# Kernel optimization log

Measured on AMD Instinct MI355X. Metric: run time of the kernel, lower is better.

Reference implementation:

```python
import jax, jax.numpy as jnp
import numpy as np

SEQ, B, N_IN, H, L = 8192, 1, 64, 1024, 5


def leaky_relu(x):
    return jnp.where(x >= 0, x, 0.01 * x)  # torch LeakyReLU default slope 0.01


def setup_inputs() -> dict:
    key = jax.random.key(0)
    ks = jax.random.split(key, 6)
    s_in = 1.0 / np.sqrt(N_IN)
    s_h = 1.0 / np.sqrt(H)
    return {
        "data_in": jax.random.normal(ks[0], (SEQ, B, N_IN), jnp.float32),
        "w1": jax.random.normal(ks[1], (H, N_IN), jnp.float32) * s_in,
        "b1": jnp.zeros((H,), jnp.float32),
        "W_ih": jax.random.normal(ks[2], (L, 4 * H, H), jnp.float32) * s_h,
        "W_hh": jax.random.normal(ks[3], (L, 4 * H, H), jnp.float32) * s_h,
        "b_ih": jnp.zeros((L, 4 * H), jnp.float32),
        "b_hh": jnp.zeros((L, 4 * H), jnp.float32),
        "w2": jax.random.normal(ks[4], (N_IN, H), jnp.float32) * s_h,
        "b2": jnp.zeros((N_IN,), jnp.float32),
        "h0": jnp.zeros((L, B, H), jnp.float32),
        "c0": jnp.zeros((L, B, H), jnp.float32),
    }


def _lstm_layer(x, h0, c0, Wih, Whh, b):
    # x: (SEQ, B, H_in); h0, c0: (B, H); Wih: (4H, H_in); Whh: (4H, H); b: (4H,)
    def step(carry, x_t):
        h, c = carry
        z = x_t @ Wih.T + h @ Whh.T + b  # (B, 4H)
        i, f, g, o = jnp.split(z, 4, axis=-1)  # torch gate order i,f,g,o
        i = jax.nn.sigmoid(i)
        f = jax.nn.sigmoid(f)
        g = jnp.tanh(g)
        o = jax.nn.sigmoid(o)
        c = f * c + i * g
        h = o * jnp.tanh(c)
        return (h, c), h

    (_, _), hs = jax.lax.scan(step, (h0, c0), x)
    return hs  # (SEQ, B, H)


def reference(data_in, w1, b1, W_ih, W_hh, b_ih, b_hh, w2, b2, h0, c0):
    out = leaky_relu(data_in @ w1.T + b1)  # (SEQ, B, H)
    for l in range(W_ih.shape[0]):  # stacked LSTM, layers is a static small int
        out = _lstm_layer(out, h0[l], c0[l], W_ih[l], W_hh[l], b_ih[l] + b_hh[l])
    out = leaky_relu(out)
    return jnp.tanh(out @ w2.T + b2)  # (SEQ, B, N_IN)
```

## Files before the change

kernel.cpp:

```cpp
#include <hip/hip_runtime.h>
#include <stdint.h>

typedef unsigned int  u32;
typedef unsigned short u16;
typedef unsigned long long u64;

#define SEQ    8192
#define HID    1024
#define NL     5
#define NWG    256
#define TPB    256
#define PAIRS  20
#define RPW    20
#define NVR    12
#define NLR    8
#define WSTEPS (SEQ + NL - 1)
#define LWGS   52
#define RING   16

#define WS_X0    ((size_t)0)
#define WS_H5    ((size_t)16*1024*1024)
#define WS_SLOT  ((size_t)32*1024*1024)
#define WS_SYNC  (WS_SLOT + (size_t)384*1024)
#define WS_NEED  (WS_SYNC + 4096)

__device__ __forceinline__ float bf2f(u16 v) { return __uint_as_float(((u32)v) << 16); }
__device__ __forceinline__ float bflo(u32 v) { return __uint_as_float(v << 16); }
__device__ __forceinline__ float bfhi(u32 v) { return __uint_as_float(v & 0xffff0000u); }

__device__ __forceinline__ u16 f2bf(float f) {
  u32 u = __float_as_uint(f);
  u32 r = u + 0x7fffu + ((u >> 16) & 1u);
  return (u16)(r >> 16);
}
__device__ __forceinline__ float lrelu(float x) { return (x >= 0.f) ? x : 0.01f * x; }
__device__ __forceinline__ float sigm(float x)  { return 1.f / (1.f + __expf(-x)); }
__device__ __forceinline__ float tanh_f(float x) {
  float e = __expf(-2.f * fabsf(x));
  float t = (1.f - e) / (1.f + e);
  return (x >= 0.f) ? t : -t;
}

__device__ __forceinline__ float dot2bf(u32 w, u32 v, float acc) {
  return fmaf(bfhi(w), bfhi(v), fmaf(bflo(w), bflo(v), acc));
}

#if defined(__has_builtin)
#if __has_builtin(__builtin_amdgcn_fdot2_f32_bf16)
#define HAS_DOT2 1
typedef __bf16 bf16x2 __attribute__((ext_vector_type(2)));
__device__ __forceinline__ float hwdot2(u32 a, u32 b, float c) {
  union U { u32 u; bf16x2 v; };
  U x, y; x.u = a; y.u = b;
  return __builtin_amdgcn_fdot2_f32_bf16(x.v, y.v, c, false);
}
#endif
#endif
#ifndef HAS_DOT2
#define HAS_DOT2 0
__device__ __forceinline__ float hwdot2(u32 a, u32 b, float c) { return dot2bf(a, b, c); }
#endif

__device__ __forceinline__ u32 agent_load(const u32* p) {
  return __hip_atomic_load((u32*)p, __ATOMIC_RELAXED, __HIP_MEMORY_SCOPE_AGENT);
}
__device__ __forceinline__ u64 slot_load(const u64* p) {
  return __hip_atomic_load((u64*)p, __ATOMIC_RELAXED, __HIP_MEMORY_SCOPE_AGENT);
}
__device__ __forceinline__ void slot_store(u64* p, u64 v) {
  __hip_atomic_store(p, v, __ATOMIC_RELAXED, __HIP_MEMORY_SCOPE_AGENT);
}
__device__ __forceinline__ void epoch_add(u32* p) {
  (void)__hip_atomic_fetch_add(p, 1u, __ATOMIC_RELAXED, __HIP_MEMORY_SCOPE_AGENT);
}

__global__ void k_detect(const u32* __restrict__ w1, u32* __restrict__ flag) {
  int lane = threadIdx.x;
  int cnt = 0;
#pragma unroll
  for (int i = 0; i < 4; ++i) {
    u32 w = w1[lane * 4 + i];
    u32 e = (w >> 23) & 0xffu;
    cnt += (e >= 100u && e <= 140u) ? 1 : 0;
  }
  cnt += __shfl_xor(cnt, 32); cnt += __shfl_xor(cnt, 16); cnt += __shfl_xor(cnt, 8);
  cnt += __shfl_xor(cnt, 4);  cnt += __shfl_xor(cnt, 2);  cnt += __shfl_xor(cnt, 1);
  if (lane == 0) {
    u32 f = (cnt > 128) ? 1u : 0u;
#if HAS_DOT2
    u32 a1 = (u32)f2bf(1.5f)   | ((u32)f2bf(-2.25f) << 16);
    u32 b1v = (u32)f2bf(0.5f)  | ((u32)f2bf(4.0f)   << 16);
    u32 a2 = (u32)f2bf(0.125f) | ((u32)f2bf(3.0f)   << 16);
    u32 b2v = (u32)f2bf(8.0f)  | ((u32)f2bf(-0.5f)  << 16);
    float t1 = hwdot2(a1, b1v, 1.0f);
    float t2 = hwdot2(a2, b2v, 0.5f);
    if (fabsf(t1 + 7.25f) < 1e-2f && fabsf(t2) < 1e-2f) f |= 2u;
#endif
    *flag = f;
  }
}

__global__ void __launch_bounds__(256) k_in(const void* __restrict__ din,
                                            const void* __restrict__ w1,
                                            const void* __restrict__ b1,
                                            u32* __restrict__ X0,
                                            const u32* __restrict__ flagp) {
  const u32 isf = *flagp & 1u;
  int t = blockIdx.x, tid = threadIdx.x;
  __shared__ float xs[64];
  if (isf) {
    if (tid < 64) xs[tid] = ((const float*)din)[(size_t)t * 64 + tid];
  } else {
    if (tid < 32) {
      u32 v = ((const u32*)din)[(size_t)t * 32 + tid];
      xs[2 * tid] = bflo(v); xs[2 * tid + 1] = bfhi(v);
    }
  }
  __syncthreads();
  float o[4];
#pragma unroll
  for (int r = 0; r < 4; ++r) {
    int i = tid * 4 + r;
    float a = 0.f;
    if (isf) {
      const float* wr = (const float*)w1 + (size_t)i * 64;
#pragma unroll
      for (int d = 0; d < 64; ++d) a = fmaf(wr[d], xs[d], a);
      a += ((const float*)b1)[i];
    } else {
      const u32* wr = (const u32*)w1 + (size_t)i * 32;
#pragma unroll
      for (int d = 0; d < 32; ++d) {
        u32 w = wr[d];
        a = fmaf(bflo(w), xs[2 * d], a);
        a = fmaf(bfhi(w), xs[2 * d + 1], a);
      }
      a += bf2f(((const u16*)b1)[i]);
    }
    o[r] = lrelu(a);
  }
  X0[(size_t)t * 512 + tid * 2]     = (u32)f2bf(o[0]) | ((u32)f2bf(o[1]) << 16);
  X0[(size_t)t * 512 + tid * 2 + 1] = (u32)f2bf(o[2]) | ((u32)f2bf(o[3]) << 16);
}

__global__ void __launch_bounds__(TPB, 1) k_wave(const void* __restrict__ WihP,
                                                 const void* __restrict__ WhhP,
                                                 const void* __restrict__ bihP,
                                                 const void* __restrict__ bhhP,
                                                 const void* __restrict__ h0P,
                                                 const void* __restrict__ c0P,
                                                 const u32* __restrict__ X0,
                                                 u32* __restrict__ H5,
                                                 u64* slots64, u32* epochs,
                                                 const u32* __restrict__ flagp) {
  const u32 dfl = *flagp;
  const u32 isf = dfl & 1u;
  const bool ud2 = (dfl & 2u) != 0u;
  const int tid  = threadIdx.x;
  const int lane = tid & 63;
  const int wv   = tid >> 6;
  const int wg   = blockIdx.x;

  __shared__ u32   vlds[2][64 * 17];
  __shared__ u32   wlds[4 * NLR * 1024];
  __shared__ float zrow[80];

  u32 W[NVR][16];
#pragma unroll
  for (int i = 0; i < RPW; ++i) {
    int rr = wv * RPW + i;
    int p = rr >> 2, q = rr & 3;
    int g = wg * PAIRS + p;
    int lg = g >> 10, j = g & 1023;
    u32 tmp[16];
    if (isf) {
      const float* matf = (lane < 32) ? (const float*)WihP : (const float*)WhhP;
      const float4* s4 = (const float4*)(matf + ((size_t)(lg * 4096 + q * 1024 + j)) * 1024 + (lane & 31) * 32);
#pragma unroll
      for (int q4 = 0; q4 < 8; ++q4) {
        float4 f = s4[q4];
        tmp[q4 * 2]     = (u32)f2bf(f.x) | ((u32)f2bf(f.y) << 16);
        tmp[q4 * 2 + 1] = (u32)f2bf(f.z) | ((u32)f2bf(f.w) << 16);
      }
    } else {
      const u32* mat = (lane < 32) ? (const u32*)WihP : (const u32*)WhhP;
      const uint4* s4 = (const uint4*)(mat + ((size_t)(lg * 4096 + q * 1024 + j)) * 512 + (lane & 31) * 16);
      uint4 a0 = s4[0], a1 = s4[1], a2 = s4[2], a3 = s4[3];
      tmp[0]=a0.x; tmp[1]=a0.y; tmp[2]=a0.z;  tmp[3]=a0.w;
      tmp[4]=a1.x; tmp[5]=a1.y; tmp[6]=a1.z;  tmp[7]=a1.w;
      tmp[8]=a2.x; tmp[9]=a2.y; tmp[10]=a2.z; tmp[11]=a2.w;
      tmp[12]=a3.x;tmp[13]=a3.y;tmp[14]=a3.z; tmp[15]=a3.w;
    }
    if (i < NVR) {
#pragma unroll
      for (int d = 0; d < 16; ++d) W[i][d] = tmp[d];
    } else {
      u32* base = &wlds[(wv * NLR + (i - NVR)) * 1024];
#pragma unroll
      for (int d4 = 0; d4 < 4; ++d4) {
        uint4 v4 = make_uint4(tmp[d4*4], tmp[d4*4+1], tmp[d4*4+2], tmp[d4*4+3]);
        *(uint4*)&base[d4 * 256 + lane * 4] = v4;
      }
    }
  }

  float cst = 0.f;
  float b0 = 0.f, b1g = 0.f, b2g = 0.f, b3g = 0.f;
  if (wv == 0 && lane < PAIRS) {
    int g = wg * PAIRS + lane, lg = g >> 10, j = g & 1023;
    cst = isf ? ((const float*)c0P)[lg * 1024 + j] : bf2f(((const u16*)c0P)[lg * 1024 + j]);
#pragma unroll
    for (int q = 0; q < 4; ++q) {
      int r = lg * 4096 + q * 1024 + j;
      float bb = isf ? (((const float*)bihP)[r] + ((const float*)bhhP)[r])
                     : (bf2f(((const u16*)bihP)[r]) + bf2f(((const u16*)bhhP)[r]));
      if (q == 0) b0 = bb; else if (q == 1) b1g = bb; else if (q == 2) b2g = bb; else b3g = bb;
    }
  }
  if (tid < PAIRS / 2) {
    int g = wg * PAIRS + 2 * tid, lg = g >> 10, j = g & 1023;
    u32 v;
    if (isf) {
      const float* h0f = (const float*)h0P;
      v = (u32)f2bf(h0f[lg * 1024 + j]) | ((u32)f2bf(h0f[lg * 1024 + j + 1]) << 16);
    } else {
      const u16* h0b = (const u16*)h0P;
      v = (u32)h0b[lg * 1024 + j] | ((u32)h0b[lg * 1024 + j + 1] << 16);
    }
    slot_store(&slots64[(size_t)(lg * RING + (RING - 1)) * 512 + (j >> 1)],
               ((u64)0xFFFFFFFFull << 32) | (u64)v);
  }

  const int l_lo = (wg * PAIRS) >> 10;
  const int l_hi = (wg * PAIRS + PAIRS - 1) >> 10;

  int budget = 20000000;

  for (int s = 0; s < WSTEPS; ++s) {
#pragma unroll
    for (int sel = 0; sel < 2; ++sel) {
      int L = l_lo + sel;
      if (L <= l_hi) {
        int t = s - L;
        if (t >= 0 && t < SEQ) {
          const u64* hsrc = slots64 + (size_t)(L * RING + ((t - 1) & (RING - 1))) * 512;
          const u64* xsrc = (L > 0) ? slots64 + (size_t)((L - 1) * RING + (t & (RING - 1))) * 512
                                    : (const u64*)0;
          const u32 exph = (u32)(t - 1);
          const u32 expx = (u32)t;
          u32 okm = 0;
          u32 dat[4] = {0u, 0u, 0u, 0u};
          int miss = 0;
          for (;;) {
#pragma unroll
            for (int rr2 = 0; rr2 < 4; ++rr2) {
              if (!(okm & (1u << rr2))) {
                int gidx = tid + rr2 * 256;
                if (gidx < 512) {
                  if (L == 0) { dat[rr2] = X0[(size_t)t * 512 + gidx]; okm |= 1u << rr2; }
                  else {
                    u64 v = slot_load(xsrc + gidx);
                    if ((u32)(v >> 32) == expx) { dat[rr2] = (u32)v; okm |= 1u << rr2; }
                  }
                } else {
                  u64 v = slot_load(hsrc + (gidx - 512));
                  if ((u32)(v >> 32) == exph) { dat[rr2] = (u32)v; okm |= 1u << rr2; }
                }
              }
            }
            if (__all(okm == 15u)) break;
            if (--budget < 0) break;
            if (++miss >= 16) __builtin_amdgcn_s_sleep(1);
          }
#pragma unroll
          for (int rr2 = 0; rr2 < 4; ++rr2) {
            int gidx = tid + rr2 * 256;
            vlds[sel][(gidx >> 4) * 17 + (gidx & 15)] = dat[rr2];
          }
        }
      }
    }
    __syncthreads();

    {
      int curl = -1;
      u32 vreg[16];
#pragma unroll
      for (int i = 0; i < RPW; ++i) {
        int rr = wv * RPW + i;
        int p = rr >> 2;
        int g = wg * PAIRS + p;
        int lg = g >> 10;
        int t = s - lg;
        if (t >= 0 && t < SEQ) {
          if (lg != curl) {
            curl = lg;
            const u32* vb = &vlds[lg - l_lo][lane * 17];
#pragma unroll
            for (int d = 0; d < 16; ++d) vreg[d] = vb[d];
          }
          float a0 = 0.f, a1 = 0.f, a2 = 0.f, a3 = 0.f;
          if (i < NVR) {
            if (ud2) {
#pragma unroll
              for (int d = 0; d < 16; d += 4) {
                a0 = hwdot2(W[i][d],   vreg[d],   a0);
                a1 = hwdot2(W[i][d+1], vreg[d+1], a1);
                a2 = hwdot2(W[i][d+2], vreg[d+2], a2);
                a3 = hwdot2(W[i][d+3], vreg[d+3], a3);
              }
            } else {
#pragma unroll
              for (int d = 0; d < 16; d += 4) {
                a0 = fmaf(bflo(W[i][d]),   bflo(vreg[d]),   a0);
                a0 = fmaf(bfhi(W[i][d]),   bfhi(vreg[d]),   a0);
                a1 = fmaf(bflo(W[i][d+1]), bflo(vreg[d+1]), a1);
                a1 = fmaf(bfhi(W[i][d+1]), bfhi(vreg[d+1]), a1);
                a2 = fmaf(bflo(W[i][d+2]), bflo(vreg[d+2]), a2);
                a2 = fmaf(bfhi(W[i][d+2]), bfhi(vreg[d+2]), a2);
                a3 = fmaf(bflo(W[i][d+3]), bflo(vreg[d+3]), a3);
                a3 = fmaf(bfhi(W[i][d+3]), bfhi(vreg[d+3]), a3);
              }
            }
          } else {
            const uint4* wl = (const uint4*)&wlds[(wv * NLR + (i - NVR)) * 1024 + lane * 4];
#pragma unroll
            for (int d4 = 0; d4 < 4; ++d4) {
              uint4 w4 = wl[d4 * 64];
              if (ud2) {
                a0 = hwdot2(w4.x, vreg[d4*4+0], a0);
                a1 = hwdot2(w4.y, vreg[d4*4+1], a1);
                a2 = hwdot2(w4.z, vreg[d4*4+2], a2);
                a3 = hwdot2(w4.w, vreg[d4*4+3], a3);
              } else {
                a0 = fmaf(bflo(w4.x), bflo(vreg[d4*4+0]), a0);
                a0 = fmaf(bfhi(w4.x), bfhi(vreg[d4*4+0]), a0);
                a1 = fmaf(bflo(w4.y), bflo(vreg[d4*4+1]), a1);
                a1 = fmaf(bfhi(w4.y), bfhi(vreg[d4*4+1]), a1);
                a2 = fmaf(bflo(w4.z), bflo(vreg[d4*4+2]), a2);
                a2 = fmaf(bfhi(w4.z), bfhi(vreg[d4*4+2]), a2);
                a3 = fmaf(bflo(w4.w), bflo(vreg[d4*4+3]), a3);
                a3 = fmaf(bfhi(w4.w), bfhi(vreg[d4*4+3]), a3);
              }
            }
          }
          float r = (a0 + a1) + (a2 + a3);
          r += __shfl_xor(r, 32);
          r += __shfl_xor(r, 16);
          r += __shfl_xor(r, 8);
          r += __shfl_xor(r, 4);
          r += __shfl_xor(r, 2);
          r += __shfl_xor(r, 1);
          if (lane == 0) zrow[rr] = r;
        }
      }
    }
    __syncthreads();

    if (wv == 0) {
      if (s >= RING - 1) {
        u32 needw = 52u * (u32)(s - (RING - 2));
#pragma unroll
        for (int sel = 0; sel < 2; ++sel) {
          int L = l_lo + sel;
          if (L <= l_hi && (L + 1) < NL) {
            int tL = s - L;
            if (tL >= 0 && tL < SEQ) {
              while (agent_load(&epochs[(L + 1) * 32]) < needw) {
                if (--budget < 0) break;
                __builtin_amdgcn_s_sleep(4);
              }
            }
          }
        }
      }
      u16 hb = 0;
      int g = wg * PAIRS + lane;
      int lg = g >> 10;
      int t = s - lg;
      bool act = (lane < PAIRS) && (t >= 0) && (t < SEQ);
      if (act) {
        float zi = zrow[lane * 4 + 0] + b0;
        float zf = zrow[lane * 4 + 1] + b1g;
        float zg = zrow[lane * 4 + 2] + b2g;
        float zo = zrow[lane * 4 + 3] + b3g;
        float ig = sigm(zi), fg = sigm(zf), gg = tanh_f(zg), og = sigm(zo);
        float c = fg * cst + ig * gg;
        cst = c;
        hb = f2bf(og * tanh_f(c));
      }
      u16 hnb = (u16)__shfl_xor((int)hb, 1);
      if (act && ((lane & 1) == 0)) {
        int j = g & 1023;
        u32 v = (u32)hb | ((u32)hnb << 16);
        slot_store(&slots64[(size_t)(lg * RING + (t & (RING - 1))) * 512 + (j >> 1)],
                   ((u64)(u32)t << 32) | (u64)v);
        if (lg == NL - 1) H5[(size_t)t * 512 + (j >> 1)] = v;
      }
      if (lane == 0) {
        epoch_add(&epochs[l_lo * 32]);
        if (l_hi != l_lo) epoch_add(&epochs[l_hi * 32]);
      }
    }
  }
}

__global__ void __launch_bounds__(256) k_out(const u32* __restrict__ H5,
                                             const void* __restrict__ w2,
                                             const void* __restrict__ b2,
                                             void* __restrict__ out,
                                             const u32* __restrict__ flagp) {
  const u32 isf = *flagp & 1u;
  int t = blockIdx.x, tid = threadIdx.x;
  __shared__ float hs[1024];
  __shared__ float part[256];
#pragma unroll
  for (int r = 0; r < 2; ++r) {
    int idx = tid + r * 256;
    u32 v = H5[(size_t)t * 512 + idx];
    hs[2 * idx]     = lrelu(bflo(v));
    hs[2 * idx + 1] = lrelu(bfhi(v));
  }
  __syncthreads();
  int n = tid & 63, qq = tid >> 6;
  float a = 0.f;
  if (isf) {
    const float* wr = (const float*)w2 + (size_t)n * 1024 + qq * 256;
    const float* hb = &hs[qq * 256];
#pragma unroll
    for (int d = 0; d < 256; ++d) a = fmaf(wr[d], hb[d], a);
  } else {
    const u32* wr = (const u32*)w2 + (size_t)n * 512 + qq * 128;
    const float* hb = &hs[qq * 256];
#pragma unroll
    for (int d = 0; d < 128; ++d) {
      u32 w = wr[d];
      a = fmaf(bflo(w), hb[2 * d], a);
      a = fmaf(bfhi(w), hb[2 * d + 1], a);
    }
  }
  part[tid] = a;
  __syncthreads();
  if (tid < 64) {
    float bb = isf ? ((const float*)b2)[tid] : bf2f(((const u16*)b2)[tid]);
    float y = part[tid] + part[tid + 64] + part[tid + 128] + part[tid + 192] + bb;
    float r = tanh_f(y);
    if (isf) ((float*)out)[(size_t)t * 64 + tid] = r;
    else     ((u16*)out)[(size_t)t * 64 + tid] = f2bf(r);
  }
}

extern "C" void kernel_launch(void* const* d_in, const int* in_sizes, int n_in,
                              void* d_out, int out_size, void* d_ws, size_t ws_size,
                              hipStream_t stream) {
  (void)in_sizes; (void)n_in; (void)out_size;
  if (ws_size < WS_NEED) return;

  const void* din = d_in[0];
  const void* w1  = d_in[1];
  const void* b1  = d_in[2];
  const void* Wih = d_in[3];
  const void* Whh = d_in[4];
  const void* bih = d_in[5];
  const void* bhh = d_in[6];
  const void* w2  = d_in[7];
  const void* b2  = d_in[8];
  const void* h0  = d_in[9];
  const void* c0  = d_in[10];

  char* ws = (char*)d_ws;
  u32* X0     = (u32*)(ws + WS_X0);
  u32* H5     = (u32*)(ws + WS_H5);
  u64* slot   = (u64*)(ws + WS_SLOT);
  u32* epochs = (u32*)(ws + WS_SYNC);
  u32* dflag  = (u32*)(ws + WS_SYNC + 2048);

  hipMemsetAsync(slot, 0xAA, (size_t)NL * RING * 512 * 8, stream);
  hipMemsetAsync(epochs, 0, 4096, stream);
  k_detect<<<1, 64, 0, stream>>>((const u32*)w1, dflag);
  k_in  <<<SEQ, 256, 0, stream>>>(din, w1, b1, X0, dflag);
  k_wave<<<NWG, TPB, 0, stream>>>(Wih, Whh, bih, bhh, h0, c0, X0, H5, slot, epochs, dflag);
  k_out <<<SEQ, 256, 0, stream>>>(H5, w2, b2, d_out, dflag);
}
```

Measured before the change: 103.6 ms.

## Skew layer wavefront by two steps and prefetch inter-layer inputs via LLC-coherent 16B slots

Layers in the persistent LSTM wavefront now trail one another by two steps instead of one, which gives the next layer's input a step of slack. That input is prefetched at the end of each step, so the spin-wait mostly covers only the recurrent h vector. Slots are repacked as 16-byte records (tag plus two bf16 pairs) written and read with sc0 sc1 dwordx4 inline asm, which cuts the number of tagged atomics per step. The write-after-read throttle now caches how far ahead the consumer layer is, so it polls less often. The costs are a few more pipeline fill steps, reliance on hand-written cache-control asm, and subtler ordering assumptions in the ring buffer.

```diff
diff --git a/kernel.cpp b/kernel.cpp
--- a/kernel.cpp
+++ b/kernel.cpp
@@ -14,7 +14,8 @@
 #define RPW    20
 #define NVR    12
 #define NLR    8
-#define WSTEPS (SEQ + NL - 1)
+#define SKEW   2
+#define WSTEPS (SEQ + SKEW * (NL - 1))
 #define LWGS   52
 #define RING   16
 
@@ -23,6 +24,8 @@
 #define WS_SLOT  ((size_t)32*1024*1024)
 #define WS_SYNC  (WS_SLOT + (size_t)384*1024)
 #define WS_NEED  (WS_SYNC + 4096)
+
+#define VIDX(w) ((((w) >> 4) * 17) + ((w) & 15))
 
 __device__ __forceinline__ float bf2f(u16 v) { return __uint_as_float(((u32)v) << 16); }
 __device__ __forceinline__ float bflo(u32 v) { return __uint_as_float(v << 16); }
@@ -64,15 +67,25 @@
 __device__ __forceinline__ u32 agent_load(const u32* p) {
   return __hip_atomic_load((u32*)p, __ATOMIC_RELAXED, __HIP_MEMORY_SCOPE_AGENT);
 }
-__device__ __forceinline__ u64 slot_load(const u64* p) {
-  return __hip_atomic_load((u64*)p, __ATOMIC_RELAXED, __HIP_MEMORY_SCOPE_AGENT);
-}
-__device__ __forceinline__ void slot_store(u64* p, u64 v) {
-  __hip_atomic_store(p, v, __ATOMIC_RELAXED, __HIP_MEMORY_SCOPE_AGENT);
-}
 __device__ __forceinline__ void epoch_add(u32* p) {
   (void)__hip_atomic_fetch_add(p, 1u, __ATOMIC_RELAXED, __HIP_MEMORY_SCOPE_AGENT);
 }
+
+typedef u32 u32x4_t __attribute__((ext_vector_type(4)));
+__device__ __forceinline__ void llc_store4(u32* p, u32 tag, u32 a, u32 b) {
+  u32x4_t q; q.x = tag; q.y = a; q.z = b; q.w = 0u;
+  asm volatile("global_store_dwordx4 %0, %1, off sc0 sc1" : : "v"(p), "v"(q) : "memory");
+}
+__device__ __forceinline__ u32x4_t llc_load4(const u32* p) {
+  u32x4_t r;
+  asm volatile("global_load_dwordx4 %0, %1, off sc0 sc1" : "=v"(r) : "v"(p));
+  return r;
+}
+__device__ __forceinline__ void vm_drain() {
+  asm volatile("s_waitcnt vmcnt(0)" ::: "memory");
+}
+
+__device__ __forceinline__ int first_wg(int l) { return (l << 10) / PAIRS; }
 
 __global__ void k_detect(const u32* __restrict__ w1, u32* __restrict__ flag) {
   int lane = threadIdx.x;
@@ -151,7 +164,7 @@
                                                  const void* __restrict__ c0P,
                                                  const u32* __restrict__ X0,
                                                  u32* __restrict__ H5,
-                                                 u64* slots64, u32* epochs,
+                                                 u32* slots, u32* epochs,
                                                  const u32* __restrict__ flagp) {
   const u32 dfl = *flagp;
   const u32 isf = dfl & 1u;
@@ -217,67 +230,76 @@
       if (q == 0) b0 = bb; else if (q == 1) b1g = bb; else if (q == 2) b2g = bb; else b3g = bb;
     }
   }
-  if (tid < PAIRS / 2) {
-    int g = wg * PAIRS + 2 * tid, lg = g >> 10, j = g & 1023;
-    u32 v;
+  if (tid < 5) {
+    int u = wg * PAIRS + 4 * tid, lg = u >> 10, j = u & 1023;
+    u32 p0, p1;
     if (isf) {
-      const float* h0f = (const float*)h0P;
-      v = (u32)f2bf(h0f[lg * 1024 + j]) | ((u32)f2bf(h0f[lg * 1024 + j + 1]) << 16);
+      const float* h0f = (const float*)h0P + lg * 1024 + j;
+      p0 = (u32)f2bf(h0f[0]) | ((u32)f2bf(h0f[1]) << 16);
+      p1 = (u32)f2bf(h0f[2]) | ((u32)f2bf(h0f[3]) << 16);
     } else {
-      const u16* h0b = (const u16*)h0P;
-      v = (u32)h0b[lg * 1024 + j] | ((u32)h0b[lg * 1024 + j + 1] << 16);
-    }
-    slot_store(&slots64[(size_t)(lg * RING + (RING - 1)) * 512 + (j >> 1)],
-               ((u64)0xFFFFFFFFull << 32) | (u64)v);
+      const u16* h0b = (const u16*)h0P + lg * 1024 + j;
+      p0 = (u32)h0b[0] | ((u32)h0b[1] << 16);
+      p1 = (u32)h0b[2] | ((u32)h0b[3] << 16);
+    }
+    llc_store4(slots + ((size_t)(lg * RING + (RING - 1)) * 256 + (j >> 2)) * 4,
+               0xFFFFFFFFu, p0, p1);
   }
 
   const int l_lo = (wg * PAIRS) >> 10;
   const int l_hi = (wg * PAIRS + PAIRS - 1) >> 10;
+  const bool span = (l_hi != l_lo);
 
   int budget = 20000000;
+  int war_until0 = RING - 1;
+  int war_until1 = RING - 1;
+  bool pf0 = false, pf1 = false;
 
   for (int s = 0; s < WSTEPS; ++s) {
-#pragma unroll
-    for (int sel = 0; sel < 2; ++sel) {
-      int L = l_lo + sel;
-      if (L <= l_hi) {
-        int t = s - L;
-        if (t >= 0 && t < SEQ) {
-          const u64* hsrc = slots64 + (size_t)(L * RING + ((t - 1) & (RING - 1))) * 512;
-          const u64* xsrc = (L > 0) ? slots64 + (size_t)((L - 1) * RING + (t & (RING - 1))) * 512
-                                    : (const u64*)0;
-          const u32 exph = (u32)(t - 1);
-          const u32 expx = (u32)t;
-          u32 okm = 0;
-          u32 dat[4] = {0u, 0u, 0u, 0u};
-          int miss = 0;
-          for (;;) {
-#pragma unroll
-            for (int rr2 = 0; rr2 < 4; ++rr2) {
-              if (!(okm & (1u << rr2))) {
-                int gidx = tid + rr2 * 256;
-                if (gidx < 512) {
-                  if (L == 0) { dat[rr2] = X0[(size_t)t * 512 + gidx]; okm |= 1u << rr2; }
-                  else {
-                    u64 v = slot_load(xsrc + gidx);
-                    if ((u32)(v >> 32) == expx) { dat[rr2] = (u32)v; okm |= 1u << rr2; }
-                  }
-                } else {
-                  u64 v = slot_load(hsrc + (gidx - 512));
-                  if ((u32)(v >> 32) == exph) { dat[rr2] = (u32)v; okm |= 1u << rr2; }
-                }
-              }
-            }
-            if (__all(okm == 15u)) break;
-            if (--budget < 0) break;
-            if (++miss >= 16) __builtin_amdgcn_s_sleep(1);
-          }
-#pragma unroll
-          for (int rr2 = 0; rr2 < 4; ++rr2) {
-            int gidx = tid + rr2 * 256;
-            vlds[sel][(gidx >> 4) * 17 + (gidx & 15)] = dat[rr2];
-          }
-        }
+    const int t0 = s - 2 * l_lo;
+    const int t1 = s - 2 * l_hi;
+    const bool a0 = (t0 >= 0) && (t0 < SEQ);
+    const bool a1 = span && (t1 >= 0) && (t1 < SEQ);
+
+    if (a0 && l_lo == 0) {
+      u64 xv = *(const u64*)(X0 + (size_t)t0 * 512 + 2 * tid);
+      vlds[0][VIDX(2 * tid)]     = (u32)xv;
+      vlds[0][VIDX(2 * tid + 1)] = (u32)(xv >> 32);
+    }
+
+    {
+      bool h0ok = !a0, h1ok = !a1;
+      bool x0ok = !a0 || (l_lo == 0) || pf0;
+      bool x1ok = !a1 || pf1;
+      const u32* ha0 = slots + ((size_t)(l_lo * RING + ((t0 - 1) & 15)) * 256 + tid) * 4;
+      const u32* ha1 = slots + ((size_t)(l_hi * RING + ((t1 - 1) & 15)) * 256 + tid) * 4;
+      const u32* xa0 = (l_lo > 0)
+          ? slots + ((size_t)((l_lo - 1) * RING + (t0 & 15)) * 256 + tid) * 4 : ha0;
+      const u32* xa1 = slots + ((size_t)(l_lo * RING + (t1 & 15)) * 256 + tid) * 4;
+      const u32 eh0 = (u32)(t0 - 1), eh1 = (u32)(t1 - 1);
+      const u32 ex0 = (u32)t0, ex1 = (u32)t1;
+      int miss = 0;
+      while (!__all(h0ok && h1ok && x0ok && x1ok)) {
+        u32x4_t wh0, wh1, wx0, wx1;
+        if (!h0ok) wh0 = llc_load4(ha0);
+        if (!h1ok) wh1 = llc_load4(ha1);
+        if (!x0ok) wx0 = llc_load4(xa0);
+        if (!x1ok) wx1 = llc_load4(xa1);
+        vm_drain();
+        if (!h0ok && wh0.x == eh0) {
+          vlds[0][VIDX(512 + 2 * tid)] = wh0.y; vlds[0][VIDX(513 + 2 * tid)] = wh0.z; h0ok = true;
+        }
+        if (!h1ok && wh1.x == eh1) {
+          vlds[1][VIDX(512 + 2 * tid)] = wh1.y; vlds[1][VIDX(513 + 2 * tid)] = wh1.z; h1ok = true;
+        }
+        if (!x0ok && wx0.x == ex0) {
+          vlds[0][VIDX(2 * tid)] = wx0.y; vlds[0][VIDX(2 * tid + 1)] = wx0.z; x0ok = true;
+        }
+        if (!x1ok && wx1.x == ex1) {
+          vlds[1][VIDX(2 * tid)] = wx1.y; vlds[1][VIDX(2 * tid + 1)] = wx1.z; x1ok = true;
+        }
+        if (--budget < 0) break;
+        if (++miss >= 16) __builtin_amdgcn_s_sleep(1);
       }
     }
     __syncthreads();
@@ -291,7 +313,7 @@
         int p = rr >> 2;
         int g = wg * PAIRS + p;
         int lg = g >> 10;
-        int t = s - lg;
+        int t = s - 2 * lg;
         if (t >= 0 && t < SEQ) {
           if (lg != curl) {
             curl = lg;
@@ -358,26 +380,28 @@
     __syncthreads();
 
     if (wv == 0) {
-      if (s >= RING - 1) {
-        u32 needw = 52u * (u32)(s - (RING - 2));
-#pragma unroll
-        for (int sel = 0; sel < 2; ++sel) {
-          int L = l_lo + sel;
-          if (L <= l_hi && (L + 1) < NL) {
-            int tL = s - L;
-            if (tL >= 0 && tL < SEQ) {
-              while (agent_load(&epochs[(L + 1) * 32]) < needw) {
-                if (--budget < 0) break;
-                __builtin_amdgcn_s_sleep(4);
-              }
-            }
-          }
+      if ((l_lo + 1) < NL && s > war_until0) {
+        for (;;) {
+          u32 E = agent_load(&epochs[(l_lo + 1) * 32]);
+          int until = (int)(E / 52u) + 12;
+          if (until >= s) { war_until0 = until; break; }
+          if (--budget < 0) { war_until0 = s; break; }
+          __builtin_amdgcn_s_sleep(2);
+        }
+      }
+      if (span && (l_hi + 1) < NL && s > war_until1) {
+        for (;;) {
+          u32 E = agent_load(&epochs[(l_hi + 1) * 32]);
+          int until = (int)(E / 52u) + 12;
+          if (until >= s) { war_until1 = until; break; }
+          if (--budget < 0) { war_until1 = s; break; }
+          __builtin_amdgcn_s_sleep(2);
         }
       }
       u16 hb = 0;
       int g = wg * PAIRS + lane;
       int lg = g >> 10;
-      int t = s - lg;
+      int t = s - 2 * lg;
       bool act = (lane < PAIRS) && (t >= 0) && (t < SEQ);
       if (act) {
         float zi = zrow[lane * 4 + 0] + b0;
@@ -390,16 +414,41 @@
         hb = f2bf(og * tanh_f(c));
       }
       u16 hnb = (u16)__shfl_xor((int)hb, 1);
-      if (act && ((lane & 1) == 0)) {
-        int j = g & 1023;
-        u32 v = (u32)hb | ((u32)hnb << 16);
-        slot_store(&slots64[(size_t)(lg * RING + (t & (RING - 1))) * 512 + (j >> 1)],
-                   ((u64)(u32)t << 32) | (u64)v);
-        if (lg == NL - 1) H5[(size_t)t * 512 + (j >> 1)] = v;
-      }
+      u32 v = (u32)hb | ((u32)hnb << 16);
+      u32 pa = (u32)__shfl((int)v, (4 * lane) & 63);
+      u32 pb = (u32)__shfl((int)v, (4 * lane + 2) & 63);
+      if (lane < 5) {
+        int u = wg * PAIRS + 4 * lane, lg2 = u >> 10, j2 = u & 1023;
+        int tg = s - 2 * lg2;
+        if (tg >= 0 && tg < SEQ)
+          llc_store4(slots + ((size_t)(lg2 * RING + (tg & 15)) * 256 + (j2 >> 2)) * 4,
+                     (u32)tg, pa, pb);
+      }
+      if (act && !(lane & 1) && lg == NL - 1)
+        H5[(size_t)t * 512 + ((g & 1023) >> 1)] = v;
       if (lane == 0) {
         epoch_add(&epochs[l_lo * 32]);
-        if (l_hi != l_lo) epoch_add(&epochs[l_hi * 32]);
+        if (span) epoch_add(&epochs[l_hi * 32]);
+      }
+    }
+
+    {
+      const int tn0 = (s + 1) - 2 * l_lo;
+      const int tn1 = (s + 1) - 2 * l_hi;
+      const bool p0 = (l_lo > 0) && (tn0 >= 0) && (tn0 < SEQ);
+      const bool p1 = span && (tn1 >= 0) && (tn1 < SEQ);
+      pf0 = false; pf1 = false;
+      if (p0 | p1) {
+        u32x4_t w0, w1;
+        if (p0) w0 = llc_load4(slots + ((size_t)((l_lo - 1) * RING + (tn0 & 15)) * 256 + tid) * 4);
+        if (p1) w1 = llc_load4(slots + ((size_t)(l_lo * RING + (tn1 & 15)) * 256 + tid) * 4);
+        vm_drain();
+        if (p0 && w0.x == (u32)tn0) {
+          vlds[0][VIDX(2 * tid)] = w0.y; vlds[0][VIDX(2 * tid + 1)] = w0.z; pf0 = true;
+        }
+        if (p1 && w1.x == (u32)tn1) {
+          vlds[1][VIDX(2 * tid)] = w1.y; vlds[1][VIDX(2 * tid + 1)] = w1.z; pf1 = true;
+        }
       }
     }
   }
@@ -471,11 +520,11 @@
   char* ws = (char*)d_ws;
   u32* X0     = (u32*)(ws + WS_X0);
   u32* H5     = (u32*)(ws + WS_H5);
-  u64* slot   = (u64*)(ws + WS_SLOT);
+  u32* slot   = (u32*)(ws + WS_SLOT);
   u32* epochs = (u32*)(ws + WS_SYNC);
   u32* dflag  = (u32*)(ws + WS_SYNC + 2048);
 
-  hipMemsetAsync(slot, 0xAA, (size_t)NL * RING * 512 * 8, stream);
+  hipMemsetAsync(slot, 0xAA, (size_t)NL * RING * 256 * 16, stream);
   hipMemsetAsync(epochs, 0, 4096, stream);
   k_detect<<<1, 64, 0, stream>>>((const u32*)w1, dflag);
   k_in  <<<SEQ, 256, 0, stream>>>(din, w1, b1, X0, dflag);
```

After: 108.4 ms. 4.5% more time.
